# Kernel optimization log

Measured on AMD Instinct MI355X. Metric: run time of the kernel, lower is better.

## Reference

```python
import jax, jax.numpy as jnp
import numpy as np

D_IN = 1024
D_OUT = 1024
N_HEADS = 16
HEAD_DIM = D_OUT // N_HEADS


def setup_inputs() -> dict:
    key = jax.random.key(0)
    ks = jax.random.split(key, 6)
    s = 0.02
    x = jax.random.normal(ks[0], (4, 2048, D_IN), dtype=jnp.float32)
    Wq = jax.random.normal(ks[1], (D_IN, D_OUT), dtype=jnp.float32) * s
    Wk = jax.random.normal(ks[2], (D_IN, D_OUT), dtype=jnp.float32) * s
    Wv = jax.random.normal(ks[3], (D_IN, D_OUT), dtype=jnp.float32) * s
    Wo = jax.random.normal(ks[4], (D_OUT, D_OUT), dtype=jnp.float32) * s
    bo = jax.random.normal(ks[5], (D_OUT,), dtype=jnp.float32) * s
    return {"x": x, "Wq": Wq, "Wk": Wk, "Wv": Wv, "Wo": Wo, "bo": bo}


def reference(x, Wq, Wk, Wv, Wo, bo):
    B, S, _ = x.shape
    # projections -> [B, H, S, Dh]
    def split_heads(t):
        return t.reshape(B, S, N_HEADS, HEAD_DIM).transpose(0, 2, 1, 3)
    q = split_heads(x @ Wq)
    k = split_heads(x @ Wk)
    v = split_heads(x @ Wv)
    scores = jnp.einsum('bhqd,bhkd->bhqk', q, k)  # [B,H,S,S]
    causal = jnp.triu(jnp.ones((S, S), dtype=bool), k=1)
    scores = jnp.where(causal, -jnp.inf, scores)
    attn = jax.nn.softmax(scores / np.sqrt(HEAD_DIM).astype(np.float32), axis=-1)
    ctx = jnp.einsum('bhqk,bhkd->bhqd', attn, v)  # [B,H,S,Dh]
    ctx = ctx.transpose(0, 2, 1, 3).reshape(B, S, D_OUT)
    return ctx @ Wo + bo
```

## Files before the change

kernel.cpp:

```cpp
#include <hip/hip_runtime.h>
#include <hip/hip_bf16.h>
#include <math.h>

typedef __attribute__((ext_vector_type(8))) short bf16x8;
typedef __attribute__((ext_vector_type(4))) float f32x4;
typedef __attribute__((ext_vector_type(16))) float f32x16;
typedef __attribute__((ext_vector_type(4))) unsigned int u32x4;

static constexpr int Mtot = 8192;
static constexpr int Dmod = 1024;
static constexpr int SEQ  = 2048;
static constexpr int NH   = 16;
static constexpr int DH   = 64;

static constexpr float QSCALE = 0.18033688011112042f;

__device__ __forceinline__ unsigned short f2bf(float x) {
    unsigned int u = __float_as_uint(x);
    u += 0x7fff + ((u >> 16) & 1);
    return (unsigned short)(u >> 16);
}

__device__ __forceinline__ float bf2f(short s) {
    return __uint_as_float(((unsigned int)(unsigned short)s) << 16);
}

__device__ __forceinline__ void gload_lds16(const void* g, void* l) {
    __builtin_amdgcn_global_load_lds(
        (const __attribute__((address_space(1))) unsigned int*)g,
        (__attribute__((address_space(3))) unsigned int*)l, 16, 0, 0);
}

__global__ __launch_bounds__(256)
void cvt_bf16(const float* __restrict__ in, unsigned short* __restrict__ out, int n4) {
    int i = blockIdx.x * blockDim.x + threadIdx.x;
    const int stride = gridDim.x * blockDim.x;
    for (; i < n4; i += stride) {
        float4 v = ((const float4*)in)[i];
        ushort4 o;
        o.x = f2bf(v.x); o.y = f2bf(v.y); o.z = f2bf(v.z); o.w = f2bf(v.w);
        ((ushort4*)out)[i] = o;
    }
}

__global__ __launch_bounds__(256)
void transpose_cvt4(const float* __restrict__ W0, const float* __restrict__ W1,
                    const float* __restrict__ W2, const float* __restrict__ W3,
                    unsigned short* __restrict__ T0, unsigned short* __restrict__ T1,
                    unsigned short* __restrict__ T2, unsigned short* __restrict__ T3) {
    __shared__ float tile[64][68];
    const int z = blockIdx.z;
    const float* W = z == 0 ? W0 : z == 1 ? W1 : z == 2 ? W2 : W3;
    unsigned short* Wt = z == 0 ? T0 : z == 1 ? T1 : z == 2 ? T2 : T3;

    const int n0 = blockIdx.x * 64, k0 = blockIdx.y * 64;
    const int t = threadIdx.x;
    const int r = t >> 4, c4 = (t & 15) * 4;
#pragma unroll
    for (int i = 0; i < 4; ++i) {
        float4 v = *(const float4*)&W[(size_t)(k0 + r + i * 16) * Dmod + n0 + c4];
        tile[c4 + 0][r + i * 16] = v.x;
        tile[c4 + 1][r + i * 16] = v.y;
        tile[c4 + 2][r + i * 16] = v.z;
        tile[c4 + 3][r + i * 16] = v.w;
    }
    __syncthreads();
#pragma unroll
    for (int i = 0; i < 4; ++i) {
        ushort4 o;
        o.x = f2bf(tile[r + i * 16][c4 + 0]);
        o.y = f2bf(tile[r + i * 16][c4 + 1]);
        o.z = f2bf(tile[r + i * 16][c4 + 2]);
        o.w = f2bf(tile[r + i * 16][c4 + 3]);
        *(ushort4*)&Wt[(size_t)(n0 + r + i * 16) * Dmod + k0 + c4] = o;
    }
}

template<int MODE>
__global__ __launch_bounds__(512)
void gemm256(const unsigned short* __restrict__ A,
             const unsigned short* __restrict__ Bw,
             const float* __restrict__ bias,
             unsigned short* __restrict__ Qb,
             unsigned short* __restrict__ Kb,
             unsigned short* __restrict__ Vtb,
             float* __restrict__ Fout) {
    constexpr int MF   = 4;
    constexpr int AHB  = 8192;
    constexpr int OFF_A0 = 0, OFF_B0 = AHB, OFF_A1 = AHB + 16384, OFF_B1 = 2 * AHB + 16384;
    constexpr int BUFB = 2 * AHB + 32768;
    constexpr int NTN  = MODE == 0 ? 12 : 4;
    constexpr int MPX  = 8;

    __shared__ __align__(16) char lds[2 * BUFB];

    const int id  = blockIdx.x;
    const int xcd = id & 7, idx = id >> 3;
    const int mt = xcd * MPX + idx / NTN;
    const int nt = idx % NTN;
    const int m0 = mt * 128, n0 = nt * 256;

    const int t = threadIdx.x;
    const int wid = t >> 6, l = t & 63;
    const int wm = wid >> 2, wn = wid & 3;
    const int r16 = l & 15, g = l >> 4;

    auto stageA = [&](int kt, int kh, int regionOff) {
        char* dst = lds + regionOff + wid * 1024;
        const int o  = t * 16;
        const int lg = o ^ (((o >> 7) & 3) << 4);
        gload_lds16((const char*)A + (size_t)(m0 + (lg >> 6)) * 2048
                        + kt * 128 + kh * 64 + (lg & 63),
                    dst);
    };
    auto stageB = [&](int kt, int kh, int regionOff) {
        char* dst = lds + regionOff + wid * 1024;
#pragma unroll
        for (int r = 0; r < 2; ++r) {
            const int o  = r * 8192 + t * 16;
            const int lg = o ^ (((o >> 7) & 3) << 4);
            gload_lds16((const char*)Bw + (size_t)(n0 + (lg >> 6)) * 2048
                            + kt * 128 + kh * 64 + (lg & 63),
                        dst + r * 8192);
        }
    };

    f32x4 acc[MF][4];
    const f32x4 z = {0.f, 0.f, 0.f, 0.f};
#pragma unroll
    for (int i = 0; i < MF; ++i)
#pragma unroll
        for (int j = 0; j < 4; ++j) acc[i][j] = z;

    stageA(0, 0, OFF_A0);
    stageB(0, 0, OFF_B0);
    stageA(0, 1, OFF_A1);
    stageB(0, 1, OFF_B1);

    const int arow0 = wm * (MF * 16) + r16;
    const int brow0 = wn * 64 + r16;
    const int gb = g * 16;

    auto gate = [&]() {
        asm volatile("s_waitcnt vmcnt(4)" ::: "memory");
        __builtin_amdgcn_s_barrier();
    };

    for (int kt = 0; kt < 16; ++kt) {
        const int buf  = (kt & 1) * BUFB;
        const int nbuf = buf ^ BUFB;
        const int ktn  = kt < 15 ? kt + 1 : 15;
        bf16x8 af[MF], bv[2];

        stageA(ktn, 0, nbuf + OFF_A0);
        gate();
#pragma unroll
        for (int mi = 0; mi < MF; ++mi) {
            const int row = arow0 + mi * 16;
            af[mi] = *(const bf16x8*)(lds + buf + OFF_A0
                      + ((row * 64 + gb) ^ (((row >> 1) & 3) << 4)));
        }
#pragma unroll
        for (int ni = 0; ni < 2; ++ni) {
            const int row = brow0 + ni * 16;
            bv[ni] = *(const bf16x8*)(lds + buf + OFF_B0
                      + ((row * 64 + gb) ^ (((row >> 1) & 3) << 4)));
        }
        asm volatile("s_waitcnt lgkmcnt(0)" ::: "memory");
        __builtin_amdgcn_sched_barrier(0);
        __builtin_amdgcn_s_setprio(1);
#pragma unroll
        for (int mi = 0; mi < MF; ++mi)
#pragma unroll
            for (int ni = 0; ni < 2; ++ni)
                acc[mi][ni] = __builtin_amdgcn_mfma_f32_16x16x32_bf16(
                    af[mi], bv[ni], acc[mi][ni], 0, 0, 0);
        __builtin_amdgcn_s_setprio(0);

        stageB(ktn, 0, nbuf + OFF_B0);
#pragma unroll
        for (int ni = 0; ni < 2; ++ni) {
            const int row = brow0 + (2 + ni) * 16;
            bv[ni] = *(const bf16x8*)(lds + buf + OFF_B0
                      + ((row * 64 + gb) ^ (((row >> 1) & 3) << 4)));
        }
        asm volatile("s_waitcnt lgkmcnt(0)" ::: "memory");
        __builtin_amdgcn_sched_barrier(0);
        __builtin_amdgcn_s_setprio(1);
#pragma unroll
        for (int mi = 0; mi < MF; ++mi)
#pragma unroll
            for (int ni = 0; ni < 2; ++ni)
                acc[mi][2 + ni] = __builtin_amdgcn_mfma_f32_16x16x32_bf16(
                    af[mi], bv[ni], acc[mi][2 + ni], 0, 0, 0);
        __builtin_amdgcn_s_setprio(0);

        stageA(ktn, 1, nbuf + OFF_A1);
        gate();
#pragma unroll
        for (int mi = 0; mi < MF; ++mi) {
            const int row = arow0 + mi * 16;
            af[mi] = *(const bf16x8*)(lds + buf + OFF_A1
                      + ((row * 64 + gb) ^ (((row >> 1) & 3) << 4)));
        }
#pragma unroll
        for (int ni = 0; ni < 2; ++ni) {
            const int row = brow0 + ni * 16;
            bv[ni] = *(const bf16x8*)(lds + buf + OFF_B1
                      + ((row * 64 + gb) ^ (((row >> 1) & 3) << 4)));
        }
        asm volatile("s_waitcnt lgkmcnt(0)" ::: "memory");
        __builtin_amdgcn_sched_barrier(0);
        __builtin_amdgcn_s_setprio(1);
#pragma unroll
        for (int mi = 0; mi < MF; ++mi)
#pragma unroll
            for (int ni = 0; ni < 2; ++ni)
                acc[mi][ni] = __builtin_amdgcn_mfma_f32_16x16x32_bf16(
                    af[mi], bv[ni], acc[mi][ni], 0, 0, 0);
        __builtin_amdgcn_s_setprio(0);

        stageB(ktn, 1, nbuf + OFF_B1);
#pragma unroll
        for (int ni = 0; ni < 2; ++ni) {
            const int row = brow0 + (2 + ni) * 16;
            bv[ni] = *(const bf16x8*)(lds + buf + OFF_B1
                      + ((row * 64 + gb) ^ (((row >> 1) & 3) << 4)));
        }
        asm volatile("s_waitcnt lgkmcnt(0)" ::: "memory");
        __builtin_amdgcn_sched_barrier(0);
        __builtin_amdgcn_s_setprio(1);
#pragma unroll
        for (int mi = 0; mi < MF; ++mi)
#pragma unroll
            for (int ni = 0; ni < 2; ++ni)
                acc[mi][2 + ni] = __builtin_amdgcn_mfma_f32_16x16x32_bf16(
                    af[mi], bv[ni], acc[mi][2 + ni], 0, 0, 0);
        __builtin_amdgcn_s_setprio(0);
    }

    if constexpr (MODE == 0) {
        const int region = n0 >> 10;
        if (region <= 1) {
            unsigned short* outp = region ? Kb : Qb;
            const float qs = region == 0 ? QSCALE : 1.0f;
#pragma unroll
            for (int mi = 0; mi < MF; ++mi) {
                const int mrow = m0 + wm * (MF * 16) + mi * 16 + g * 4;
#pragma unroll
                for (int ni = 0; ni < 4; ++ni) {
                    const int ncol = (n0 & 1023) + wn * 64 + ni * 16 + r16;
#pragma unroll
                    for (int reg = 0; reg < 4; ++reg)
                        outp[(size_t)(mrow + reg) * Dmod + ncol] = f2bf(acc[mi][ni][reg] * qs);
                }
            }
        } else {
#pragma unroll
            for (int mi = 0; mi < MF; ++mi) {
                const int mrow = m0 + wm * (MF * 16) + mi * 16 + g * 4;
                const int bidx = mrow >> 11, s = mrow & 2047;
#pragma unroll
                for (int ni = 0; ni < 4; ++ni) {
                    const int n = (n0 & 1023) + wn * 64 + ni * 16 + r16;
                    const int bh = bidx * NH + (n >> 6), d = n & 63;
                    ushort4 o;
                    o.x = f2bf(acc[mi][ni][0]); o.y = f2bf(acc[mi][ni][1]);
                    o.z = f2bf(acc[mi][ni][2]); o.w = f2bf(acc[mi][ni][3]);
                    *(ushort4*)&Vtb[((size_t)bh * DH + d) * SEQ + s] = o;
                }
            }
        }
    } else {
        float bb[4];
#pragma unroll
        for (int ni = 0; ni < 4; ++ni)
            bb[ni] = bias[n0 + wn * 64 + ni * 16 + r16];
#pragma unroll
        for (int mi = 0; mi < MF; ++mi) {
            const int mrow = m0 + wm * (MF * 16) + mi * 16 + g * 4;
#pragma unroll
            for (int ni = 0; ni < 4; ++ni) {
                const int ncol = n0 + wn * 64 + ni * 16 + r16;
#pragma unroll
                for (int reg = 0; reg < 4; ++reg)
                    Fout[(size_t)(mrow + reg) * Dmod + ncol] = acc[mi][ni][reg] + bb[ni];
            }
        }
    }
}

__global__ __launch_bounds__(256, 4)
void attn_mfma(const unsigned short* __restrict__ Qg,
               const unsigned short* __restrict__ Kg,
               const unsigned short* __restrict__ Vtg,
               unsigned short* __restrict__ pO,
               float* __restrict__ pL) {
    __shared__ __align__(16) short Ks[2][64 * 64];
    __shared__ __align__(16) short Vs[64 * 64];

    const int id   = blockIdx.x;
    const int xcd  = id & 7;
    const int bh   = ((id >> 7) << 3) | xcd;
    const int mid  = (id >> 3) & 15;
    const int pidx = mid >> 1;
    const int par  = mid & 1;
    const int b = bh >> 4, h = bh & 15;
    const int t = threadIdx.x, wid = t >> 6, l = t & 63;
    const int lo = l & 31, hi = l >> 5;
    const int srow8 = t >> 3, scolb = (t & 7) * 16;

    unsigned int kbase[2], vbase[2];
#pragma unroll
    for (int c = 0; c < 2; ++c) {
        const int row = c * 32 + srow8;
        const int swz = scolb ^ ((row & 7) << 4);
        kbase[c] = (unsigned int)(((b * SEQ + row) * Dmod + h * DH) * 2 + swz);
        vbase[c] = (unsigned int)(((bh * DH + row) * SEQ) * 2 + swz);
    }

    auto stageK = [&](int jt, int buf) {
#pragma unroll
        for (int c = 0; c < 2; ++c)
            gload_lds16((const char*)Kg + kbase[c] + ((size_t)jt << 17),
                        (char*)&Ks[buf][0] + c * 4096 + wid * 1024);
    };
    auto stageV = [&](int jt) {
#pragma unroll
        for (int c = 0; c < 2; ++c)
            gload_lds16((const char*)Vtg + vbase[c] + ((size_t)jt << 7),
                        (char*)&Vs[0] + c * 4096 + wid * 1024);
    };

    for (int pass = 0; pass < 2; ++pass) {
        const int qt = pass ? pidx : 15 - pidx;
        const int qw0 = qt * 128 + wid * 32;
        const int qg = qw0 + lo;
        const int jmax = 2 * qt + 1;

        __syncthreads();
        bf16x8 bq[4];
#pragma unroll
        for (int dc = 0; dc < 4; ++dc)
            bq[dc] = *(const bf16x8*)&Qg[(size_t)(b * SEQ + qg) * Dmod + h * DH + dc * 16 + 8 * hi];
        stageK(par, 0);
        stageV(par);
        __syncthreads();

        float l_run = 0.f;
        f32x16 oacc0, oacc1;
#pragma unroll
        for (int r = 0; r < 16; ++r) { oacc0[r] = 0.f; oacc1[r] = 0.f; }

        int cur = 0;
        for (int jt = par; jt <= jmax; jt += 2) {
            const bool more = (jt + 2 <= jmax);
            if (more) stageK(jt + 2, cur ^ 1);
            const char* Kc = (const char*)&Ks[cur][0];
            const char* Vc = (const char*)&Vs[0];
            const bool diag = (jt >= 2 * qt);

#pragma unroll
            for (int c32 = 0; c32 < 2; ++c32) {
                const int krow = c32 * 32 + lo;
                const int kswz = (krow & 7) << 4;
                bf16x8 ak[4];
#pragma unroll
                for (int dc = 0; dc < 4; ++dc)
                    ak[dc] = *(const bf16x8*)(Kc + krow * 128 + ((dc * 32 + 16 * hi) ^ kswz));
                f32x16 st;
#pragma unroll
                for (int r = 0; r < 16; ++r) st[r] = 0.f;
                __builtin_amdgcn_s_setprio(1);
#pragma unroll
                for (int dc = 0; dc < 4; ++dc)
                    st = __builtin_amdgcn_mfma_f32_32x32x16_bf16(ak[dc], bq[dc], st, 0, 0, 0);
                __builtin_amdgcn_s_setprio(0);

                if (diag) {
                    const int kvb = jt * 64 + c32 * 32 + 4 * hi;
#pragma unroll
                    for (int r = 0; r < 16; ++r)
                        if (kvb + (r & 3) + 8 * (r >> 2) > qg) st[r] = -INFINITY;
                }

                bf16x8 paf[2];
                float s = 0.f;
#pragma unroll
                for (int kb = 0; kb < 2; ++kb) {
                    float p[8];
#pragma unroll
                    for (int r = 0; r < 8; ++r) p[r] = exp2f(st[kb * 8 + r] - 4.0f);
                    s += ((p[0] + p[1]) + (p[2] + p[3])) + ((p[4] + p[5]) + (p[6] + p[7]));
                    unsigned int x, zz, y, w;
                    asm("v_cvt_pk_bf16_f32 %0, %1, %2" : "=v"(x)  : "v"(p[0]), "v"(p[1]));
                    asm("v_cvt_pk_bf16_f32 %0, %1, %2" : "=v"(zz) : "v"(p[2]), "v"(p[3]));
                    asm("v_cvt_pk_bf16_f32 %0, %1, %2" : "=v"(y)  : "v"(p[4]), "v"(p[5]));
                    asm("v_cvt_pk_bf16_f32 %0, %1, %2" : "=v"(w)  : "v"(p[6]), "v"(p[7]));
                    asm volatile("v_permlane32_swap_b32 %0, %1" : "+v"(x),  "+v"(y));
                    asm volatile("v_permlane32_swap_b32 %0, %1" : "+v"(zz), "+v"(w));
                    u32x4 aw; aw[0] = x; aw[1] = zz; aw[2] = y; aw[3] = w;
                    paf[kb] = __builtin_bit_cast(bf16x8, aw);
                }
                s += __shfl_xor(s, 32);
                l_run += s;

                if (c32 == 0) {
                    if (more) { asm volatile("s_waitcnt vmcnt(2)" ::: "memory"); }
                    else      { asm volatile("s_waitcnt vmcnt(0)" ::: "memory"); }
                    __builtin_amdgcn_s_barrier();
                }

#pragma unroll
                for (int kb = 0; kb < 2; ++kb) {
                    const int vbyte = c32 * 64 + kb * 32 + 16 * hi;
                    const int row0 = lo, row1 = 32 + lo;
                    const bf16x8 vb0 = *(const bf16x8*)(Vc + row0 * 128 + (vbyte ^ ((row0 & 7) << 4)));
                    const bf16x8 vb1 = *(const bf16x8*)(Vc + row1 * 128 + (vbyte ^ ((row1 & 7) << 4)));
                    __builtin_amdgcn_s_setprio(1);
                    oacc0 = __builtin_amdgcn_mfma_f32_32x32x16_bf16(paf[kb], vb0, oacc0, 0, 0, 0);
                    oacc1 = __builtin_amdgcn_mfma_f32_32x32x16_bf16(paf[kb], vb1, oacc1, 0, 0, 0);
                    __builtin_amdgcn_s_setprio(0);
                }
            }

            asm volatile("s_waitcnt vmcnt(0)" ::: "memory");
            __builtin_amdgcn_s_barrier();
            if (more) stageV(jt + 2);
            cur ^= 1;
        }

        if (hi == 0) pL[(size_t)(par * 64 + bh) * SEQ + qg] = l_run;
        const size_t pbase = (size_t)(par * 64 + bh) * SEQ;
#pragma unroll
        for (int rq = 0; rq < 4; ++rq)
#pragma unroll
            for (int e = 0; e < 4; ++e) {
                const int qrow = qw0 + 8 * rq + 4 * hi + e;
                unsigned short* pr = &pO[(pbase + qrow) * 64];
                pr[lo]      = f2bf(oacc0[rq * 4 + e]);
                pr[lo + 32] = f2bf(oacc1[rq * 4 + e]);
            }
    }
}

__global__ __launch_bounds__(256)
void attn_merge(const unsigned short* __restrict__ pO,
                const float* __restrict__ pL,
                unsigned short* __restrict__ Ctx) {
    const int gid = blockIdx.x * 256 + threadIdx.x;
    const int row = gid >> 3;
    const int d8  = (gid & 7) * 8;
    const float l0 = pL[row];
    const float l1 = pL[131072 + row];
    const float inv = 1.0f / fmaxf(l0 + l1, 1e-30f);
    const bf16x8 o0 = *(const bf16x8*)&pO[(size_t)row * 64 + d8];
    const bf16x8 o1 = *(const bf16x8*)&pO[((size_t)131072 + row) * 64 + d8];
    const int bh = row >> 11, q = row & 2047;
    unsigned short* dst = &Ctx[((size_t)((bh >> 4) * SEQ + q)) * Dmod + (bh & 15) * DH + d8];
    unsigned short r8[8];
#pragma unroll
    for (int j = 0; j < 8; ++j)
        r8[j] = f2bf((bf2f(o0[j]) + bf2f(o1[j])) * inv);
    *(ushort4*)dst       = make_ushort4(r8[0], r8[1], r8[2], r8[3]);
    *(ushort4*)(dst + 4) = make_ushort4(r8[4], r8[5], r8[6], r8[7]);
}

extern "C" void kernel_launch(void* const* d_in, const int* in_sizes, int n_in,
                              void* d_out, int out_size, void* d_ws, size_t ws_size,
                              hipStream_t stream) {
    const float* x  = (const float*)d_in[0];
    const float* Wq = (const float*)d_in[1];
    const float* Wk = (const float*)d_in[2];
    const float* Wv = (const float*)d_in[3];
    const float* Wo = (const float*)d_in[4];
    const float* bo = (const float*)d_in[5];
    float* out = (float*)d_out;

    const size_t MD = (size_t)Mtot * Dmod;
    const size_t DD = (size_t)Dmod * Dmod;
    unsigned short* xb  = (unsigned short*)d_ws;
    unsigned short* wtq = xb  + MD;
    unsigned short* wtk = wtq + DD;
    unsigned short* wtv = wtk + DD;
    unsigned short* wto = wtv + DD;
    unsigned short* Qb  = wto + DD;
    unsigned short* Kb  = Qb  + MD;
    unsigned short* Vtb = Kb  + MD;
    unsigned short* Cx  = Vtb + MD;

    unsigned short* pO = Cx + MD;
    float*          pL = (float*)(pO + (size_t)2 * 64 * SEQ * 64);

    cvt_bf16<<<2048, 256, 0, stream>>>(x, xb, (int)(MD / 4));
    transpose_cvt4<<<dim3(16, 16, 4), 256, 0, stream>>>(Wq, Wk, Wv, Wo,
                                                        wtq, wtk, wtv, wto);

    gemm256<0><<<768, 512, 0, stream>>>(xb, wtq, nullptr, Qb, Kb, Vtb, nullptr);

    attn_mfma<<<1024, 256, 0, stream>>>(Qb, Kb, Vtb, pO, pL);
    attn_merge<<<4096, 256, 0, stream>>>(pO, pL, Cx);

    gemm256<1><<<256, 512, 0, stream>>>(Cx, wto, bo, nullptr, nullptr, nullptr, out);
}
```

Measured before the change: 176.8 us.

## Split attention KV loop three ways instead of two and merge three partials

Attention work is split across three KV-tile residues (stride 3) instead of two, raising the grid from 1024 to 1536 blocks and the launch-bounds occupancy hint from 4 to 6. The merge kernel now sums three partial outputs and three row sums. The third partial buffer reuses the start of the workspace, where the bf16 copy of x lives and is no longer needed. This adds partial-write and merge traffic, and the higher occupancy hint may force register spilling.

```diff
diff --git a/kernel.cpp b/kernel.cpp
--- a/kernel.cpp
+++ b/kernel.cpp
@@ -290,21 +290,24 @@
     }
 }
 
-__global__ __launch_bounds__(256, 4)
+__global__ __launch_bounds__(256, 6)
 void attn_mfma(const unsigned short* __restrict__ Qg,
                const unsigned short* __restrict__ Kg,
                const unsigned short* __restrict__ Vtg,
-               unsigned short* __restrict__ pO,
+               unsigned short* __restrict__ pO0,
+               unsigned short* __restrict__ pO1,
+               unsigned short* __restrict__ pO2,
                float* __restrict__ pL) {
     __shared__ __align__(16) short Ks[2][64 * 64];
     __shared__ __align__(16) short Vs[64 * 64];
 
     const int id   = blockIdx.x;
     const int xcd  = id & 7;
-    const int bh   = ((id >> 7) << 3) | xcd;
-    const int mid  = (id >> 3) & 15;
-    const int pidx = mid >> 1;
-    const int par  = mid & 1;
+    const int rest = id >> 3;
+    const int bh   = ((rest / 24) << 3) | xcd;
+    const int mid  = rest % 24;
+    const int pidx = mid / 3;
+    const int e    = mid % 3;
     const int b = bh >> 4, h = bh & 15;
     const int t = threadIdx.x, wid = t >> 6, l = t & 63;
     const int lo = l & 31, hi = l >> 5;
@@ -332,6 +335,8 @@
                         (char*)&Vs[0] + c * 4096 + wid * 1024);
     };
 
+    unsigned short* const pO = e == 0 ? pO0 : (e == 1 ? pO1 : pO2);
+
     for (int pass = 0; pass < 2; ++pass) {
         const int qt = pass ? pidx : 15 - pidx;
         const int qw0 = qt * 128 + wid * 32;
@@ -343,8 +348,8 @@
 #pragma unroll
         for (int dc = 0; dc < 4; ++dc)
             bq[dc] = *(const bf16x8*)&Qg[(size_t)(b * SEQ + qg) * Dmod + h * DH + dc * 16 + 8 * hi];
-        stageK(par, 0);
-        stageV(par);
+        stageK(e, 0);
+        stageV(e);
         __syncthreads();
 
         float l_run = 0.f;
@@ -353,9 +358,9 @@
         for (int r = 0; r < 16; ++r) { oacc0[r] = 0.f; oacc1[r] = 0.f; }
 
         int cur = 0;
-        for (int jt = par; jt <= jmax; jt += 2) {
-            const bool more = (jt + 2 <= jmax);
-            if (more) stageK(jt + 2, cur ^ 1);
+        for (int jt = e; jt <= jmax; jt += 3) {
+            const bool more = (jt + 3 <= jmax);
+            if (more) stageK(jt + 3, cur ^ 1);
             const char* Kc = (const char*)&Ks[cur][0];
             const char* Vc = (const char*)&Vs[0];
             const bool diag = (jt >= 2 * qt);
@@ -426,42 +431,46 @@
 
             asm volatile("s_waitcnt vmcnt(0)" ::: "memory");
             __builtin_amdgcn_s_barrier();
-            if (more) stageV(jt + 2);
+            if (more) stageV(jt + 3);
             cur ^= 1;
         }
 
-        if (hi == 0) pL[(size_t)(par * 64 + bh) * SEQ + qg] = l_run;
-        const size_t pbase = (size_t)(par * 64 + bh) * SEQ;
+        if (hi == 0) pL[(size_t)(e * 64 + bh) * SEQ + qg] = l_run;
+        const size_t pbase = (size_t)bh * SEQ;
 #pragma unroll
         for (int rq = 0; rq < 4; ++rq)
 #pragma unroll
-            for (int e = 0; e < 4; ++e) {
-                const int qrow = qw0 + 8 * rq + 4 * hi + e;
+            for (int ee = 0; ee < 4; ++ee) {
+                const int qrow = qw0 + 8 * rq + 4 * hi + ee;
                 unsigned short* pr = &pO[(pbase + qrow) * 64];
-                pr[lo]      = f2bf(oacc0[rq * 4 + e]);
-                pr[lo + 32] = f2bf(oacc1[rq * 4 + e]);
+                pr[lo]      = f2bf(oacc0[rq * 4 + ee]);
+                pr[lo + 32] = f2bf(oacc1[rq * 4 + ee]);
             }
     }
 }
 
 __global__ __launch_bounds__(256)
-void attn_merge(const unsigned short* __restrict__ pO,
-                const float* __restrict__ pL,
-                unsigned short* __restrict__ Ctx) {
+void attn_merge3(const unsigned short* __restrict__ pO0,
+                 const unsigned short* __restrict__ pO1,
+                 const unsigned short* __restrict__ pO2,
+                 const float* __restrict__ pL,
+                 unsigned short* __restrict__ Ctx) {
     const int gid = blockIdx.x * 256 + threadIdx.x;
     const int row = gid >> 3;
     const int d8  = (gid & 7) * 8;
     const float l0 = pL[row];
     const float l1 = pL[131072 + row];
-    const float inv = 1.0f / fmaxf(l0 + l1, 1e-30f);
-    const bf16x8 o0 = *(const bf16x8*)&pO[(size_t)row * 64 + d8];
-    const bf16x8 o1 = *(const bf16x8*)&pO[((size_t)131072 + row) * 64 + d8];
+    const float l2 = pL[262144 + row];
+    const float inv = 1.0f / fmaxf(l0 + l1 + l2, 1e-30f);
+    const bf16x8 o0 = *(const bf16x8*)&pO0[(size_t)row * 64 + d8];
+    const bf16x8 o1 = *(const bf16x8*)&pO1[(size_t)row * 64 + d8];
+    const bf16x8 o2 = *(const bf16x8*)&pO2[(size_t)row * 64 + d8];
     const int bh = row >> 11, q = row & 2047;
     unsigned short* dst = &Ctx[((size_t)((bh >> 4) * SEQ + q)) * Dmod + (bh & 15) * DH + d8];
     unsigned short r8[8];
 #pragma unroll
     for (int j = 0; j < 8; ++j)
-        r8[j] = f2bf((bf2f(o0[j]) + bf2f(o1[j])) * inv);
+        r8[j] = f2bf((bf2f(o0[j]) + bf2f(o1[j]) + bf2f(o2[j])) * inv);
     *(ushort4*)dst       = make_ushort4(r8[0], r8[1], r8[2], r8[3]);
     *(ushort4*)(dst + 4) = make_ushort4(r8[4], r8[5], r8[6], r8[7]);
 }
@@ -489,8 +498,11 @@
     unsigned short* Vtb = Kb  + MD;
     unsigned short* Cx  = Vtb + MD;
 
-    unsigned short* pO = Cx + MD;
-    float*          pL = (float*)(pO + (size_t)2 * 64 * SEQ * 64);
+    const size_t POE = (size_t)64 * SEQ * 64;
+    unsigned short* pO0 = Cx + MD;
+    unsigned short* pO1 = pO0 + POE;
+    unsigned short* pO2 = (unsigned short*)d_ws;
+    float*          pL  = (float*)(pO1 + POE);
 
     cvt_bf16<<<2048, 256, 0, stream>>>(x, xb, (int)(MD / 4));
     transpose_cvt4<<<dim3(16, 16, 4), 256, 0, stream>>>(Wq, Wk, Wv, Wo,
@@ -498,8 +510,8 @@
 
     gemm256<0><<<768, 512, 0, stream>>>(xb, wtq, nullptr, Qb, Kb, Vtb, nullptr);
 
-    attn_mfma<<<1024, 256, 0, stream>>>(Qb, Kb, Vtb, pO, pL);
-    attn_merge<<<4096, 256, 0, stream>>>(pO, pL, Cx);
+    attn_mfma<<<1536, 256, 0, stream>>>(Qb, Kb, Vtb, pO0, pO1, pO2, pL);
+    attn_merge3<<<4096, 256, 0, stream>>>(pO0, pO1, pO2, pL, Cx);
 
     gemm256<1><<<256, 512, 0, stream>>>(Cx, wto, bo, nullptr, nullptr, nullptr, out);
 }
```

Result: slower. 271.8 us (+53.8%).
